# Kernel optimization log

Hardware: AMD Instinct MI355X
Metric: run time of the kernel (lower is better)

Reference implementation:

```python
import jax, jax.numpy as jnp
import numpy as np

B, T, IN, HID = 256, 512, 1024, 1024


def setup_inputs() -> dict:
    key = jax.random.key(0)
    ks = jax.random.split(key, 9)
    s = 1.0 / np.sqrt(IN + HID)
    def lin(k):
        kw, kb = jax.random.split(k)
        W = jax.random.uniform(kw, (IN + HID, HID), jnp.float32, -s, s)
        b = jax.random.uniform(kb, (HID,), jnp.float32, -s, s)
        return W, b
    Wf, bf = lin(ks[0])
    Wi, bi = lin(ks[1])
    Wo, bo = lin(ks[2])
    Wc, bc = lin(ks[3])
    x = jax.random.normal(ks[4], (B, T, IN), jnp.float32)
    return {"x": x, "Wf": Wf, "bf": bf, "Wi": Wi, "bi": bi,
            "Wo": Wo, "bo": bo, "Wc": Wc, "bc": bc}


def reference(x, Wf, bf, Wi, bi, Wo, bo, Wc, bc):
    # x: [B, T, IN]; returns final (h, c): each [B, HID]
    batch = x.shape[0]
    hid = Wf.shape[1]

    def step(carry, xt):
        h, c = carry
        comb = jnp.concatenate([xt, h], axis=1)      # [B, IN+HID]
        i = jax.nn.sigmoid(comb @ Wi + bi)
        f = jax.nn.sigmoid(comb @ Wf + bf)
        o = jax.nn.sigmoid(comb @ Wo + bo)
        g = jnp.tanh(comb @ Wc + bc)
        c_next = f * c + i * g
        h_next = o * jnp.tanh(c_next)
        return (h_next, c_next), None

    init = (jnp.zeros((batch, hid), x.dtype), jnp.zeros((batch, hid), x.dtype))
    (h, c), _ = jax.lax.scan(step, init, jnp.swapaxes(x, 0, 1))
    return (h, c)
```

## Files before the change

### kernel.cpp

```cpp
#include <hip/hip_runtime.h>
#include <hip/hip_bf16.h>
#include <hip/hip_cooperative_groups.h>

#define B_DIM 256
#define T_DIM 512
#define IN_DIM 1024
#define HID_DIM 1024
#define BLK 16384

typedef __attribute__((ext_vector_type(8))) short bf16x8;
typedef __attribute__((ext_vector_type(4))) float f32x4;

__device__ __forceinline__ unsigned short f2bf(float v) {
  unsigned int u = __float_as_uint(v);
  unsigned int r = (u + 0x7fffu + ((u >> 16) & 1u)) >> 16;
  return (unsigned short)r;
}

typedef __attribute__((address_space(3))) unsigned int lds_uint;
typedef const __attribute__((address_space(1))) unsigned int g_uint;
__device__ __forceinline__ void gload_lds16(const void* g, void* l) {
  __builtin_amdgcn_global_load_lds((g_uint*)g, (lds_uint*)l, 16, 0, 0);
}

__device__ __forceinline__ void glds4(const unsigned char* s, unsigned char* d) {
#pragma unroll
  for (int i = 0; i < 4; ++i) gload_lds16(s + i * 1024, d + i * 1024);
}

__device__ __forceinline__ void h_load(unsigned long long (&r)[8],
                                       const unsigned char* src) {
#pragma unroll
  for (int p = 0; p < 8; ++p)
    r[p] = __hip_atomic_load((const unsigned long long*)(src + p * 512),
                             __ATOMIC_RELAXED, __HIP_MEMORY_SCOPE_AGENT);
}

__device__ __forceinline__ void h_write(unsigned long long (&r)[8],
                                        unsigned char* dst) {
#pragma unroll
  for (int p = 0; p < 8; ++p)
    *(unsigned long long*)(dst + p * 512) = r[p];
  asm volatile("s_waitcnt lgkmcnt(0)" ::: "memory");
}

__device__ __forceinline__ void spin_ge(unsigned int* p, unsigned int tgt) {
  while (__hip_atomic_fetch_add(p, 0u, __ATOMIC_RELAXED,
                                __HIP_MEMORY_SCOPE_AGENT) < tgt)
    __builtin_amdgcn_s_sleep(8);
  asm volatile("" ::: "memory");
}

__global__ void prep_pack_w(const float* __restrict__ Wi, const float* __restrict__ Wf,
                            const float* __restrict__ Wo, const float* __restrict__ Wc,
                            unsigned char* __restrict__ Wp) {
  const int bid = blockIdx.x;
  const int cb = bid >> 4, kc = bid & 15;
  const int tid = threadIdx.x;
  const int col = tid & 63;
  const int g = col >> 4, h_in = col & 15;
  const int kq = tid >> 6;
  const float* W = (g == 0) ? Wi : (g == 1) ? Wf : (g == 2) ? Wo : Wc;
  const float* src = W + (size_t)(kc * 128 + kq * 32) * HID_DIM + cb * 16 + h_in;
  unsigned char* dst = Wp + (size_t)bid * BLK;
  const unsigned int xo = (unsigned int)((col & 7) << 4);
#pragma unroll
  for (int b4 = 0; b4 < 4; ++b4) {
    unsigned short u[8];
#pragma unroll
    for (int j = 0; j < 8; ++j)
      u[j] = f2bf(src[(size_t)(b4 * 8 + j) * HID_DIM]);
    uint4 pk;
    pk.x = (unsigned)u[0] | ((unsigned)u[1] << 16);
    pk.y = (unsigned)u[2] | ((unsigned)u[3] << 16);
    pk.z = (unsigned)u[4] | ((unsigned)u[5] << 16);
    pk.w = (unsigned)u[6] | ((unsigned)u[7] << 16);
    unsigned int byte = ((unsigned int)(col * 256 + kq * 64 + b4 * 16)) ^ xo;
    *(uint4*)(dst + byte) = pk;
  }
}

__global__ void prep_bias(const float* __restrict__ bi, const float* __restrict__ bf_,
                          const float* __restrict__ bo, const float* __restrict__ bc,
                          float* __restrict__ bp) {
  int p = blockIdx.x * 256 + threadIdx.x;
  int cbb = p >> 6, col = p & 63, g = col >> 4, h_in = col & 15;
  const float* b = (g == 0) ? bi : (g == 1) ? bf_ : (g == 2) ? bo : bc;
  bp[p] = b[cbb * 16 + h_in];
}

__global__ void prep_pack_x(const float* __restrict__ x, unsigned char* __restrict__ xp) {
  const int bid = blockIdx.x;
  const int kc = bid & 7, mb = (bid >> 3) & 3, t = bid >> 5;
  const int tid = threadIdx.x;
  const int row = tid >> 2, kseg = tid & 3;
  const float* src = x + ((size_t)(mb * 64 + row) * T_DIM + t) * IN_DIM + kc * 128 + kseg * 32;
  unsigned char* dst = xp + (size_t)bid * BLK;
  const unsigned int xo = (unsigned)((row & 7) << 4);
#pragma unroll
  for (int c4 = 0; c4 < 4; ++c4) {
    float4 f0 = *(const float4*)(src + c4 * 8);
    float4 f1 = *(const float4*)(src + c4 * 8 + 4);
    uint4 pk;
    pk.x = (unsigned)f2bf(f0.x) | ((unsigned)f2bf(f0.y) << 16);
    pk.y = (unsigned)f2bf(f0.z) | ((unsigned)f2bf(f0.w) << 16);
    pk.z = (unsigned)f2bf(f1.x) | ((unsigned)f2bf(f1.y) << 16);
    pk.w = (unsigned)f2bf(f1.z) | ((unsigned)f2bf(f1.w) << 16);
    *(uint4*)(dst + (((unsigned)(row * 256 + kseg * 64 + c4 * 16)) ^ xo)) = pk;
  }
}

__global__ __launch_bounds__(512, 1) void lstm_persist(
    const unsigned char* __restrict__ xp, const unsigned char* __restrict__ Wq,
    const float* __restrict__ bp, unsigned char* hring,
    unsigned int* prodCnt, unsigned int* consCnt, float* __restrict__ out) {
  extern __shared__ unsigned char ring[];
  const int wg = blockIdx.x, mb = wg >> 6, cb = wg & 63;
  const int tid = threadIdx.x, lane = tid & 63, w = tid >> 6;
  const int wr = w >> 2, wc = w & 3;
  const int fr = lane & 15;
  const unsigned koff2 = (unsigned)((lane >> 4) << 4);

  const int erow = tid & 63, hb2 = (tid >> 6) * 2;
  float bI[2], bF[2], bO[2], bG[2];
#pragma unroll
  for (int j = 0; j < 2; ++j) {
    bI[j] = bp[cb * 64 + hb2 + j];
    bF[j] = bp[cb * 64 + 16 + hb2 + j];
    bO[j] = bp[cb * 64 + 32 + hb2 + j];
    bG[j] = bp[cb * 64 + 48 + hb2 + j];
  }
  float cr[2] = {0.f, 0.f};

  const unsigned char* WB = Wq + (size_t)(cb * 16) * BLK;
  unsigned long long hA[8], hB[8];

#pragma unroll 1
  for (int t = 0; t < T_DIM; ++t) {
    const int NC = (t == 0) ? 8 : 16;
    const unsigned char* xA =
        xp + ((size_t)(t * 4 + mb)) * (8 * BLK) + w * 4096 + lane * 16;
    const unsigned char* hSrc =
        hring + (size_t)((t + 2) % 3) * 524288 +
        (size_t)(mb * 8) * BLK + w * 4096 + lane * 8;

    f32x4 acc[2] = {{0.f, 0.f, 0.f, 0.f}, {0.f, 0.f, 0.f, 0.f}};

    auto consume = [&](int buf) {
      const unsigned char* Ab = ring + buf * 32768;
      const unsigned char* Bb = Ab + BLK;
#pragma unroll
      for (int ks = 0; ks < 4; ++ks) {
        const unsigned kb2 = (unsigned)ks * 64 + koff2;
        const unsigned r0 = (unsigned)(wr * 32 + fr), r1 = r0 + 16;
        const unsigned cl = (unsigned)(wc * 16 + fr);
        bf16x8 a0 = *(const bf16x8*)(Ab + ((r0 * 256 + kb2) ^ ((r0 & 7) << 4)));
        bf16x8 a1 = *(const bf16x8*)(Ab + ((r1 * 256 + kb2) ^ ((r1 & 7) << 4)));
        bf16x8 b0 = *(const bf16x8*)(Bb + ((cl * 256 + kb2) ^ ((cl & 7) << 4)));
        acc[0] = __builtin_amdgcn_mfma_f32_16x16x32_bf16(a0, b0, acc[0], 0, 0, 0);
        acc[1] = __builtin_amdgcn_mfma_f32_16x16x32_bf16(a1, b0, acc[1], 0, 0, 0);
      }
    };

    if (w < 4) {
#pragma unroll
      for (int c = 0; c < 3; ++c)
        glds4(xA + (size_t)c * BLK, ring + c * 32768 + (w << 12));
    } else {
#pragma unroll
      for (int c = 0; c < 3; ++c)
        glds4(WB + (size_t)c * BLK + ((w - 4) << 12) + lane * 16,
              ring + c * 32768 + BLK + ((w - 4) << 12));
    }

#pragma unroll 1
    for (int kc = 0; kc < NC; ++kc) {
      const int nx = kc + 3;
      const bool isq = nx < NC;
      if (isq && nx == 8) {
        if (lane == 0) spin_ge(&prodCnt[(t - 1) * 4 + mb], 64u);
        __builtin_amdgcn_sched_barrier(0);
      }
      if (w < 4) {
        if (isq && nx < 8)
          glds4(xA + (size_t)nx * BLK, ring + (nx & 3) * 32768 + (w << 12));
        if (kc + 1 >= 8 && kc + 1 < NC) {
          unsigned char* d = ring + ((kc + 1) & 3) * 32768 + (w << 12) + lane * 8;
          if (((kc + 1) & 1) == 0) h_write(hA, d);
          else h_write(hB, d);
        }
        if (isq && nx >= 8) {
          const unsigned char* s = hSrc + (size_t)(nx - 8) * BLK;
          if ((nx & 1) == 0) h_load(hA, s);
          else h_load(hB, s);
        }
      } else {
        if (isq)
          glds4(WB + (size_t)nx * BLK + ((w - 4) << 12) + lane * 16,
                ring + (nx & 3) * 32768 + BLK + ((w - 4) << 12));
      }
      const int ahead = NC - 1 - kc;
      if (ahead >= 3)      asm volatile("s_waitcnt vmcnt(12)" ::: "memory");
      else if (ahead == 2) asm volatile("s_waitcnt vmcnt(8)" ::: "memory");
      else if (ahead == 1) asm volatile("s_waitcnt vmcnt(4)" ::: "memory");
      else                 asm volatile("s_waitcnt vmcnt(0)" ::: "memory");
      __builtin_amdgcn_s_barrier();
      consume(kc & 3);
      __builtin_amdgcn_s_barrier();
    }

    float* gates = (float*)ring;
#pragma unroll
    for (int m = 0; m < 2; ++m)
#pragma unroll
      for (int j = 0; j < 4; ++j) {
        int row = wr * 32 + m * 16 + (lane >> 4) * 4 + j;
        int col = wc * 16 + fr;
        gates[row * 65 + col] = acc[m][j];
      }
    __syncthreads();

    float hv[2];
#pragma unroll
    for (int j = 0; j < 2; ++j) {
      int hc = hb2 + j;
      float pi = gates[erow * 65 + hc] + bI[j];
      float pf = gates[erow * 65 + 16 + hc] + bF[j];
      float po = gates[erow * 65 + 32 + hc] + bO[j];
      float pg = gates[erow * 65 + 48 + hc] + bG[j];
      float ig = 1.f / (1.f + __expf(-pi));
      float fg = 1.f / (1.f + __expf(-pf));
      float og = 1.f / (1.f + __expf(-po));
      float gg = 1.f - 2.f / (1.f + __expf(2.f * pg));
      float cn = fg * cr[j] + ig * gg;
      cr[j] = cn;
      hv[j] = og * (1.f - 2.f / (1.f + __expf(2.f * cn)));
    }

    if (t >= 3) {
      if (tid == 0) spin_ge(&consCnt[(t - 2) * 4 + mb], 64u);
      __syncthreads();
    }
    if (t < T_DIM - 1) {
      int hcg = cb * 16 + hb2;
      int kc2 = hcg >> 7, kp = hcg & 127;
      unsigned byte = ((unsigned)(erow * 256 + kp * 2)) ^ ((unsigned)((erow & 7) << 4));
      unsigned pk = (unsigned)f2bf(hv[0]) | ((unsigned)f2bf(hv[1]) << 16);
      unsigned int* hd = (unsigned int*)(hring + (size_t)(t % 3) * 524288 +
                                         (size_t)(mb * 8 + kc2) * BLK + byte);
      __hip_atomic_store(hd, pk, __ATOMIC_RELAXED, __HIP_MEMORY_SCOPE_AGENT);
    }
    asm volatile("s_waitcnt vmcnt(0)" ::: "memory");
    __syncthreads();
    if (tid == 0) {
      if (t < T_DIM - 1)
        __hip_atomic_fetch_add(&prodCnt[t * 4 + mb], 1u, __ATOMIC_RELEASE,
                               __HIP_MEMORY_SCOPE_AGENT);
      if (t >= 1)
        __hip_atomic_fetch_add(&consCnt[t * 4 + mb], 1u, __ATOMIC_RELAXED,
                               __HIP_MEMORY_SCOPE_AGENT);
    }
    if (t == T_DIM - 1) {
      size_t gidx = (size_t)(mb * 64 + erow) * HID_DIM + cb * 16 + hb2;
      *(float2*)(out + gidx) = make_float2(hv[0], hv[1]);
      *(float2*)(out + (size_t)B_DIM * HID_DIM + gidx) = make_float2(cr[0], cr[1]);
    }
  }
}

extern "C" void kernel_launch(void* const* d_in, const int* in_sizes, int n_in,
                              void* d_out, int out_size, void* d_ws, size_t ws_size,
                              hipStream_t stream) {
  (void)in_sizes; (void)n_in; (void)out_size;
  const float* x   = (const float*)d_in[0];
  const float* Wf_ = (const float*)d_in[1];
  const float* bf_ = (const float*)d_in[2];
  const float* Wi_ = (const float*)d_in[3];
  const float* bi_ = (const float*)d_in[4];
  const float* Wo_ = (const float*)d_in[5];
  const float* bo_ = (const float*)d_in[6];
  const float* Wc_ = (const float*)d_in[7];
  const float* bc_ = (const float*)d_in[8];

  unsigned char* ws = (unsigned char*)d_ws;
  unsigned char* Wp = ws;
  size_t off = 16777216;
  float* bp = (float*)(ws + off);          off += 16384;
  unsigned int* prodCnt = (unsigned int*)(ws + off); off += 8192;
  unsigned int* consCnt = (unsigned int*)(ws + off); off += 8192;
  unsigned char* hring = ws + off;         off += 3 * 524288;
  unsigned char* xpp = ws + off;           off += 268435456;
  if (ws_size < off) return;
  float* out = (float*)d_out;

  prep_pack_w<<<1024, 256, 0, stream>>>(Wi_, Wf_, Wo_, Wc_, Wp);
  prep_bias<<<16, 256, 0, stream>>>(bi_, bf_, bo_, bc_, bp);
  prep_pack_x<<<16384, 256, 0, stream>>>(x, xpp);
  hipMemsetAsync(prodCnt, 0, 16384, stream);

  hipFuncSetAttribute((const void*)lstm_persist,
                      hipFuncAttributeMaxDynamicSharedMemorySize, 131072);
  const unsigned char* a_xp = xpp;
  const unsigned char* a_wp = Wp;
  const float* a_bp = bp;
  unsigned char* a_hr = hring;
  unsigned int* a_pc = prodCnt;
  unsigned int* a_cc = consCnt;
  float* a_out = out;
  void* args[] = {&a_xp, &a_wp, &a_bp, &a_hr, &a_pc, &a_cc, &a_out};
  hipLaunchCooperativeKernel((const void*)lstm_persist, dim3(256), dim3(512),
                             args, 131072u, stream);
}
```

Baseline: 11.14 ms.

## Warp-specialize LSTM: register-resident weights, x-projection one step ahead of recurrence

Adds a new persistent kernel that splits each workgroup's waves into two roles. Four waves compute the recurrent h·W_h product, and four waves compute the next timestep's x·W_x product and hand it over through a double-buffered global gx buffer. The weight slices stay in registers for the whole run instead of being streamed from memory every step. This takes the input projection off the serial critical path, so each step's dependent work covers only the hidden-state half of K. In exchange it uses more registers, adds a global round trip for the partial gate sums, and shortens the spin sleep. The old kernel is kept as a fallback for when the workspace is too small.

```diff
diff --git a/kernel.cpp b/kernel.cpp
--- a/kernel.cpp
+++ b/kernel.cpp
@@ -1,6 +1,5 @@
 #include <hip/hip_runtime.h>
 #include <hip/hip_bf16.h>
-#include <hip/hip_cooperative_groups.h>
 
 #define B_DIM 256
 #define T_DIM 512
@@ -22,33 +21,25 @@
 __device__ __forceinline__ void gload_lds16(const void* g, void* l) {
   __builtin_amdgcn_global_load_lds((g_uint*)g, (lds_uint*)l, 16, 0, 0);
 }
-
 __device__ __forceinline__ void glds4(const unsigned char* s, unsigned char* d) {
 #pragma unroll
   for (int i = 0; i < 4; ++i) gload_lds16(s + i * 1024, d + i * 1024);
-}
-
-__device__ __forceinline__ void h_load(unsigned long long (&r)[8],
-                                       const unsigned char* src) {
-#pragma unroll
-  for (int p = 0; p < 8; ++p)
-    r[p] = __hip_atomic_load((const unsigned long long*)(src + p * 512),
-                             __ATOMIC_RELAXED, __HIP_MEMORY_SCOPE_AGENT);
-}
-
-__device__ __forceinline__ void h_write(unsigned long long (&r)[8],
-                                        unsigned char* dst) {
-#pragma unroll
-  for (int p = 0; p < 8; ++p)
-    *(unsigned long long*)(dst + p * 512) = r[p];
-  asm volatile("s_waitcnt lgkmcnt(0)" ::: "memory");
 }
 
 __device__ __forceinline__ void spin_ge(unsigned int* p, unsigned int tgt) {
   while (__hip_atomic_fetch_add(p, 0u, __ATOMIC_RELAXED,
                                 __HIP_MEMORY_SCOPE_AGENT) < tgt)
-    __builtin_amdgcn_s_sleep(8);
+    __builtin_amdgcn_s_sleep(2);
   asm volatile("" ::: "memory");
+}
+
+__device__ __forceinline__ void waitvm(int n) {
+  switch (n) {
+    case 12: asm volatile("s_waitcnt vmcnt(12)" ::: "memory"); break;
+    case 8:  asm volatile("s_waitcnt vmcnt(8)" ::: "memory"); break;
+    case 4:  asm volatile("s_waitcnt vmcnt(4)" ::: "memory"); break;
+    default: asm volatile("s_waitcnt vmcnt(0)" ::: "memory"); break;
+  }
 }
 
 __global__ void prep_pack_w(const float* __restrict__ Wi, const float* __restrict__ Wf,
@@ -110,6 +101,193 @@
   }
 }
 
+__global__ __launch_bounds__(512, 2) void lstm_ws(
+    const unsigned char* __restrict__ xp, const unsigned char* __restrict__ Wq,
+    const float* __restrict__ bp, float* gx, unsigned char* hring,
+    unsigned int* prodCnt, unsigned int* consCnt, float* __restrict__ out) {
+  extern __shared__ unsigned char ring[];
+  const int wg = blockIdx.x, mb = wg >> 6, cb = wg & 63;
+  const int tid = threadIdx.x, lane = tid & 63, w = tid >> 6;
+  const bool isH = (w < 4);
+  const int wq = w & 3;
+  const int fr = lane & 15;
+  const unsigned koff2 = (unsigned)((lane >> 4) << 4);
+  const int cl = wq * 16 + fr;
+  const int rsub = (lane >> 4) * 4;
+
+  bf16x8 Breg[8][4];
+  {
+    const int hx = isH ? 8 : 0;
+#pragma unroll
+    for (int kcl = 0; kcl < 8; ++kcl)
+#pragma unroll
+      for (int ks = 0; ks < 4; ++ks)
+        Breg[kcl][ks] = *(const bf16x8*)(
+            Wq + ((size_t)(cb * 16 + hx + kcl) << 14) +
+            (((unsigned)(cl * 256 + ks * 64 + koff2)) ^ ((unsigned)((cl & 7) << 4))));
+  }
+  const int erow = tid & 63, hb2 = (tid >> 6) * 2;
+  float bI[2], bF[2], bO[2], bG[2];
+#pragma unroll
+  for (int j = 0; j < 2; ++j) {
+    bI[j] = bp[cb * 64 + hb2 + j];
+    bF[j] = bp[cb * 64 + 16 + hb2 + j];
+    bO[j] = bp[cb * 64 + 32 + hb2 + j];
+    bG[j] = bp[cb * 64 + 48 + hb2 + j];
+  }
+  float cr[2] = {0.f, 0.f};
+
+  unsigned char* hbufs = ring;
+  unsigned char* xbufs = ring + 65536;
+  float* gates = (float*)ring;
+
+#pragma unroll 1
+  for (int t = -1; t < T_DIM; ++t) {
+    const bool hAct = isH && (t >= 1);
+    const bool xAct = (!isH) && (t < T_DIM - 1);
+
+    f32x4 acc[4] = {{0.f, 0.f, 0.f, 0.f}, {0.f, 0.f, 0.f, 0.f},
+                    {0.f, 0.f, 0.f, 0.f}, {0.f, 0.f, 0.f, 0.f}};
+    if (isH && t >= 0) {
+      const float* gt = gx + (size_t)(t & 1) * 1048576 + (size_t)wg * 4096;
+#pragma unroll
+      for (int rb = 0; rb < 4; ++rb)
+#pragma unroll
+        for (int j = 0; j < 4; ++j)
+          acc[rb][j] = gt[(rb * 16 + rsub + j) * 64 + cl];
+    }
+    if (hAct) {
+      if (lane == 0) {
+        spin_ge(&prodCnt[(t - 1) * 4 + mb], 64u);
+        (void)__hip_atomic_load(&prodCnt[(t - 1) * 4 + mb], __ATOMIC_ACQUIRE,
+                                __HIP_MEMORY_SCOPE_AGENT);
+      }
+      __builtin_amdgcn_sched_barrier(0);
+    }
+    const unsigned char* hA = hring + (size_t)((t + 2) % 3) * 524288 +
+                              (size_t)(mb * 8) * BLK + wq * 4096 + lane * 16;
+    const unsigned char* xA = xp + ((size_t)((t + 1) * 4 + mb)) * (8 * BLK) +
+                              wq * 4096 + lane * 16;
+    if (hAct) {
+#pragma unroll
+      for (int c = 0; c < 3; ++c)
+        glds4(hA + (size_t)c * BLK, hbufs + c * 16384 + wq * 4096);
+    }
+    if (xAct) {
+#pragma unroll
+      for (int c = 0; c < 3; ++c)
+        glds4(xA + (size_t)c * BLK, xbufs + c * 16384 + wq * 4096);
+    }
+#pragma unroll
+    for (int kc = 0; kc < 8; ++kc) {
+      if (kc < 5) {
+        if (hAct)
+          glds4(hA + (size_t)(kc + 3) * BLK, hbufs + ((kc + 3) & 3) * 16384 + wq * 4096);
+        if (xAct)
+          glds4(xA + (size_t)(kc + 3) * BLK, xbufs + ((kc + 3) & 3) * 16384 + wq * 4096);
+      }
+      waitvm(kc < 5 ? 12 : (kc == 5 ? 8 : (kc == 6 ? 4 : 0)));
+      __builtin_amdgcn_s_barrier();
+      if (hAct || xAct) {
+        const unsigned char* Ab = (isH ? hbufs : xbufs) + (kc & 3) * 16384;
+#pragma unroll
+        for (int ks = 0; ks < 4; ++ks) {
+          const unsigned kb2 = (unsigned)ks * 64 + koff2;
+#pragma unroll
+          for (int rb = 0; rb < 4; ++rb) {
+            const unsigned row = (unsigned)(rb * 16 + fr);
+            bf16x8 a = *(const bf16x8*)(Ab + ((row * 256 + kb2) ^ ((row & 7) << 4)));
+            acc[rb] = __builtin_amdgcn_mfma_f32_16x16x32_bf16(a, Breg[kc][ks], acc[rb], 0, 0, 0);
+          }
+        }
+      }
+      __builtin_amdgcn_s_barrier();
+    }
+
+    if (isH && t >= 0) {
+#pragma unroll
+      for (int rb = 0; rb < 4; ++rb)
+#pragma unroll
+        for (int j = 0; j < 4; ++j)
+          gates[(rb * 16 + rsub + j) * 65 + cl] = acc[rb][j];
+    }
+    if (xAct) {
+      float* gt = gx + (size_t)((t + 1) & 1) * 1048576 + (size_t)wg * 4096;
+#pragma unroll
+      for (int rb = 0; rb < 4; ++rb)
+#pragma unroll
+        for (int j = 0; j < 4; ++j)
+          __hip_atomic_store(&gt[(rb * 16 + rsub + j) * 64 + cl], acc[rb][j],
+                             __ATOMIC_RELAXED, __HIP_MEMORY_SCOPE_AGENT);
+    }
+    if (t >= 0) {
+      __syncthreads();
+      float hv[2];
+#pragma unroll
+      for (int j = 0; j < 2; ++j) {
+        int hc = hb2 + j;
+        float pi = gates[erow * 65 + hc] + bI[j];
+        float pf = gates[erow * 65 + 16 + hc] + bF[j];
+        float po = gates[erow * 65 + 32 + hc] + bO[j];
+        float pg = gates[erow * 65 + 48 + hc] + bG[j];
+        float ig = 1.f / (1.f + __expf(-pi));
+        float fg = 1.f / (1.f + __expf(-pf));
+        float og = 1.f / (1.f + __expf(-po));
+        float gg = 1.f - 2.f / (1.f + __expf(2.f * pg));
+        float cn = fg * cr[j] + ig * gg;
+        cr[j] = cn;
+        hv[j] = og * (1.f - 2.f / (1.f + __expf(2.f * cn)));
+      }
+      if (t >= 3) {
+        if (tid == 0) spin_ge(&consCnt[(t - 2) * 4 + mb], 64u);
+        __syncthreads();
+      }
+      if (t < T_DIM - 1) {
+        int hcg = cb * 16 + hb2;
+        int kc2 = hcg >> 7, kp = hcg & 127;
+        unsigned byte = ((unsigned)(erow * 256 + kp * 2)) ^ ((unsigned)((erow & 7) << 4));
+        unsigned pk = (unsigned)f2bf(hv[0]) | ((unsigned)f2bf(hv[1]) << 16);
+        unsigned int* hd = (unsigned int*)(hring + (size_t)(t % 3) * 524288 +
+                                           (size_t)(mb * 8 + kc2) * BLK + byte);
+        __hip_atomic_store(hd, pk, __ATOMIC_RELAXED, __HIP_MEMORY_SCOPE_AGENT);
+      }
+      asm volatile("s_waitcnt vmcnt(0)" ::: "memory");
+      __syncthreads();
+      if (tid == 0) {
+        if (t < T_DIM - 1)
+          __hip_atomic_fetch_add(&prodCnt[t * 4 + mb], 1u, __ATOMIC_RELEASE,
+                                 __HIP_MEMORY_SCOPE_AGENT);
+        if (t >= 1)
+          __hip_atomic_fetch_add(&consCnt[t * 4 + mb], 1u, __ATOMIC_RELAXED,
+                                 __HIP_MEMORY_SCOPE_AGENT);
+      }
+      if (t == T_DIM - 1) {
+        size_t gidx = (size_t)(mb * 64 + erow) * HID_DIM + cb * 16 + hb2;
+        *(float2*)(out + gidx) = make_float2(hv[0], hv[1]);
+        *(float2*)(out + (size_t)B_DIM * HID_DIM + gidx) = make_float2(cr[0], cr[1]);
+      }
+    } else {
+      asm volatile("s_waitcnt vmcnt(0)" ::: "memory");
+      __syncthreads();
+    }
+  }
+}
+
+__device__ __forceinline__ void h_load_fb(unsigned long long (&r)[8],
+                                          const unsigned char* src) {
+#pragma unroll
+  for (int p = 0; p < 8; ++p)
+    r[p] = __hip_atomic_load((const unsigned long long*)(src + p * 512),
+                             __ATOMIC_RELAXED, __HIP_MEMORY_SCOPE_AGENT);
+}
+__device__ __forceinline__ void h_write_fb(unsigned long long (&r)[8],
+                                           unsigned char* dst) {
+#pragma unroll
+  for (int p = 0; p < 8; ++p)
+    *(unsigned long long*)(dst + p * 512) = r[p];
+  asm volatile("s_waitcnt lgkmcnt(0)" ::: "memory");
+}
+
 __global__ __launch_bounds__(512, 1) void lstm_persist(
     const unsigned char* __restrict__ xp, const unsigned char* __restrict__ Wq,
     const float* __restrict__ bp, unsigned char* hring,
@@ -120,7 +298,6 @@
   const int wr = w >> 2, wc = w & 3;
   const int fr = lane & 15;
   const unsigned koff2 = (unsigned)((lane >> 4) << 4);
-
   const int erow = tid & 63, hb2 = (tid >> 6) * 2;
   float bI[2], bF[2], bO[2], bG[2];
 #pragma unroll
@@ -131,7 +308,6 @@
     bG[j] = bp[cb * 64 + 48 + hb2 + j];
   }
   float cr[2] = {0.f, 0.f};
-
   const unsigned char* WB = Wq + (size_t)(cb * 16) * BLK;
   unsigned long long hA[8], hB[8];
 
@@ -143,9 +319,7 @@
     const unsigned char* hSrc =
         hring + (size_t)((t + 2) % 3) * 524288 +
         (size_t)(mb * 8) * BLK + w * 4096 + lane * 8;
-
     f32x4 acc[2] = {{0.f, 0.f, 0.f, 0.f}, {0.f, 0.f, 0.f, 0.f}};
-
     auto consume = [&](int buf) {
       const unsigned char* Ab = ring + buf * 32768;
       const unsigned char* Bb = Ab + BLK;
@@ -153,15 +327,14 @@
       for (int ks = 0; ks < 4; ++ks) {
         const unsigned kb2 = (unsigned)ks * 64 + koff2;
         const unsigned r0 = (unsigned)(wr * 32 + fr), r1 = r0 + 16;
-        const unsigned cl = (unsigned)(wc * 16 + fr);
+        const unsigned clx = (unsigned)(wc * 16 + fr);
         bf16x8 a0 = *(const bf16x8*)(Ab + ((r0 * 256 + kb2) ^ ((r0 & 7) << 4)));
         bf16x8 a1 = *(const bf16x8*)(Ab + ((r1 * 256 + kb2) ^ ((r1 & 7) << 4)));
-        bf16x8 b0 = *(const bf16x8*)(Bb + ((cl * 256 + kb2) ^ ((cl & 7) << 4)));
+        bf16x8 b0 = *(const bf16x8*)(Bb + ((clx * 256 + kb2) ^ ((clx & 7) << 4)));
         acc[0] = __builtin_amdgcn_mfma_f32_16x16x32_bf16(a0, b0, acc[0], 0, 0, 0);
         acc[1] = __builtin_amdgcn_mfma_f32_16x16x32_bf16(a1, b0, acc[1], 0, 0, 0);
       }
     };
-
     if (w < 4) {
 #pragma unroll
       for (int c = 0; c < 3; ++c)
@@ -172,7 +345,6 @@
         glds4(WB + (size_t)c * BLK + ((w - 4) << 12) + lane * 16,
               ring + c * 32768 + BLK + ((w - 4) << 12));
     }
-
 #pragma unroll 1
     for (int kc = 0; kc < NC; ++kc) {
       const int nx = kc + 3;
@@ -186,13 +358,13 @@
           glds4(xA + (size_t)nx * BLK, ring + (nx & 3) * 32768 + (w << 12));
         if (kc + 1 >= 8 && kc + 1 < NC) {
           unsigned char* d = ring + ((kc + 1) & 3) * 32768 + (w << 12) + lane * 8;
-          if (((kc + 1) & 1) == 0) h_write(hA, d);
-          else h_write(hB, d);
+          if (((kc + 1) & 1) == 0) h_write_fb(hA, d);
+          else h_write_fb(hB, d);
         }
         if (isq && nx >= 8) {
           const unsigned char* s = hSrc + (size_t)(nx - 8) * BLK;
-          if ((nx & 1) == 0) h_load(hA, s);
-          else h_load(hB, s);
+          if ((nx & 1) == 0) h_load_fb(hA, s);
+          else h_load_fb(hB, s);
         }
       } else {
         if (isq)
@@ -208,7 +380,6 @@
       consume(kc & 3);
       __builtin_amdgcn_s_barrier();
     }
-
     float* gates = (float*)ring;
 #pragma unroll
     for (int m = 0; m < 2; ++m)
@@ -219,7 +390,6 @@
         gates[row * 65 + col] = acc[m][j];
       }
     __syncthreads();
-
     float hv[2];
 #pragma unroll
     for (int j = 0; j < 2; ++j) {
@@ -236,7 +406,6 @@
       cr[j] = cn;
       hv[j] = og * (1.f - 2.f / (1.f + __expf(2.f * cn)));
     }
-
     if (t >= 3) {
       if (tid == 0) spin_ge(&consCnt[(t - 2) * 4 + mb], 64u);
       __syncthreads();
@@ -281,33 +450,52 @@
   const float* bo_ = (const float*)d_in[6];
   const float* Wc_ = (const float*)d_in[7];
   const float* bc_ = (const float*)d_in[8];
-
+  float* out = (float*)d_out;
   unsigned char* ws = (unsigned char*)d_ws;
+
   unsigned char* Wp = ws;
   size_t off = 16777216;
-  float* bp = (float*)(ws + off);          off += 16384;
+  float* bp = (float*)(ws + off);                    off += 16384;
   unsigned int* prodCnt = (unsigned int*)(ws + off); off += 8192;
   unsigned int* consCnt = (unsigned int*)(ws + off); off += 8192;
-  unsigned char* hring = ws + off;         off += 3 * 524288;
-  unsigned char* xpp = ws + off;           off += 268435456;
-  if (ws_size < off) return;
-  float* out = (float*)d_out;
+  unsigned char* hring = ws + off;                   off += 3 * 524288;
+  float* gxr = (float*)(ws + off);                   off += 2 * 4194304;
+  unsigned char* xpp = ws + off;                     off += 268435456;
+  const size_t NEED_NEW = off;
 
   prep_pack_w<<<1024, 256, 0, stream>>>(Wi_, Wf_, Wo_, Wc_, Wp);
   prep_bias<<<16, 256, 0, stream>>>(bi_, bf_, bo_, bc_, bp);
-  prep_pack_x<<<16384, 256, 0, stream>>>(x, xpp);
   hipMemsetAsync(prodCnt, 0, 16384, stream);
 
-  hipFuncSetAttribute((const void*)lstm_persist,
-                      hipFuncAttributeMaxDynamicSharedMemorySize, 131072);
-  const unsigned char* a_xp = xpp;
-  const unsigned char* a_wp = Wp;
-  const float* a_bp = bp;
-  unsigned char* a_hr = hring;
-  unsigned int* a_pc = prodCnt;
-  unsigned int* a_cc = consCnt;
-  float* a_out = out;
-  void* args[] = {&a_xp, &a_wp, &a_bp, &a_hr, &a_pc, &a_cc, &a_out};
-  hipLaunchCooperativeKernel((const void*)lstm_persist, dim3(256), dim3(512),
-                             args, 131072u, stream);
-}
+  if (ws_size >= NEED_NEW) {
+    prep_pack_x<<<16384, 256, 0, stream>>>(x, xpp);
+    hipFuncSetAttribute((const void*)lstm_ws,
+                        hipFuncAttributeMaxDynamicSharedMemorySize, 131072);
+    const unsigned char* a_xp = xpp;
+    const unsigned char* a_wp = Wp;
+    const float* a_bp = bp;
+    float* a_gx = gxr;
+    unsigned char* a_hr = hring;
+    unsigned int* a_pc = prodCnt;
+    unsigned int* a_cc = consCnt;
+    float* a_out = out;
+    void* args[] = {&a_xp, &a_wp, &a_bp, &a_gx, &a_hr, &a_pc, &a_cc, &a_out};
+    hipLaunchCooperativeKernel((const void*)lstm_ws, dim3(256), dim3(512),
+                               args, 131072u, stream);
+  } else {
+    unsigned char* xpp3 = ws + (NEED_NEW - 268435456 - 2 * 4194304);
+    prep_pack_x<<<16384, 256, 0, stream>>>(x, xpp3);
+    hipFuncSetAttribute((const void*)lstm_persist,
+                        hipFuncAttributeMaxDynamicSharedMemorySize, 131072);
+    const unsigned char* a_xp = xpp3;
+    const unsigned char* a_wp = Wp;
+    const float* a_bp = bp;
+    unsigned char* a_hr = hring;
+    unsigned int* a_pc = prodCnt;
+    unsigned int* a_cc = consCnt;
+    float* a_out = out;
+    void* args[] = {&a_xp, &a_wp, &a_bp, &a_hr, &a_pc, &a_cc, &a_out};
+    hipLaunchCooperativeKernel((const void*)lstm_persist, dim3(256), dim3(512),
+                               args, 131072u, stream);
+  }
+}
```

Measured after the change: 17.79 ms. +59.7%, slower.

## Hoist input projection into windowed bulk GEMM and keep recurrent weights in registers

Applied to the files above, without the earlier changes.

Splits the LSTM into time windows. In each window a parallel bulk_gx kernel precomputes the x@W input-gate contributions for all steps and stores them as bf16. A persistent lstm_seq kernel then does only the h@W recurrent half per step, with weight slices held in registers instead of streamed from global memory every step. This removes half the serial-path GEMM work and the per-step weight traffic. In exchange it adds extra kernel launches per window, storage of precomputed gates in bf16 (more rounding), and carrying the cell state across launches.

```diff
diff --git a/kernel.cpp b/kernel.cpp
--- a/kernel.cpp
+++ b/kernel.cpp
@@ -1,9 +1,9 @@
 #include <hip/hip_runtime.h>
 #include <hip/hip_bf16.h>
-#include <hip/hip_cooperative_groups.h>
 
 #define B_DIM 256
 #define T_DIM 512
+#define WINT 64
 #define IN_DIM 1024
 #define HID_DIM 1024
 #define BLK 16384
@@ -16,40 +16,27 @@
   unsigned int r = (u + 0x7fffu + ((u >> 16) & 1u)) >> 16;
   return (unsigned short)r;
 }
+__device__ __forceinline__ float bflo(unsigned u) { return __uint_as_float(u << 16); }
+__device__ __forceinline__ float bfhi(unsigned u) { return __uint_as_float(u & 0xffff0000u); }
 
 typedef __attribute__((address_space(3))) unsigned int lds_uint;
 typedef const __attribute__((address_space(1))) unsigned int g_uint;
 __device__ __forceinline__ void gload_lds16(const void* g, void* l) {
   __builtin_amdgcn_global_load_lds((g_uint*)g, (lds_uint*)l, 16, 0, 0);
 }
-
-__device__ __forceinline__ void glds4(const unsigned char* s, unsigned char* d) {
-#pragma unroll
-  for (int i = 0; i < 4; ++i) gload_lds16(s + i * 1024, d + i * 1024);
-}
-
-__device__ __forceinline__ void h_load(unsigned long long (&r)[8],
-                                       const unsigned char* src) {
-#pragma unroll
-  for (int p = 0; p < 8; ++p)
-    r[p] = __hip_atomic_load((const unsigned long long*)(src + p * 512),
-                             __ATOMIC_RELAXED, __HIP_MEMORY_SCOPE_AGENT);
-}
-
-__device__ __forceinline__ void h_write(unsigned long long (&r)[8],
-                                        unsigned char* dst) {
-#pragma unroll
-  for (int p = 0; p < 8; ++p)
-    *(unsigned long long*)(dst + p * 512) = r[p];
-  asm volatile("s_waitcnt lgkmcnt(0)" ::: "memory");
+__device__ __forceinline__ void glds2(const unsigned char* s, unsigned char* d) {
+  gload_lds16(s, d);
+  gload_lds16(s + 1024, d + 1024);
 }
 
 __device__ __forceinline__ void spin_ge(unsigned int* p, unsigned int tgt) {
   while (__hip_atomic_fetch_add(p, 0u, __ATOMIC_RELAXED,
                                 __HIP_MEMORY_SCOPE_AGENT) < tgt)
-    __builtin_amdgcn_s_sleep(8);
+    __builtin_amdgcn_s_sleep(2);
   asm volatile("" ::: "memory");
 }
+
+#define WAITVM(N) asm volatile("s_waitcnt vmcnt(" #N ")" ::: "memory")
 
 __global__ void prep_pack_w(const float* __restrict__ Wi, const float* __restrict__ Wf,
                             const float* __restrict__ Wo, const float* __restrict__ Wc,
@@ -89,13 +76,15 @@
   bp[p] = b[cbb * 16 + h_in];
 }
 
-__global__ void prep_pack_x(const float* __restrict__ x, unsigned char* __restrict__ xp) {
+__global__ void prep_pack_x_win(const float* __restrict__ x,
+                                unsigned char* __restrict__ xpw, int t0) {
   const int bid = blockIdx.x;
-  const int kc = bid & 7, mb = (bid >> 3) & 3, t = bid >> 5;
+  const int kc = bid & 7, mb = (bid >> 3) & 3, tw = bid >> 5;
   const int tid = threadIdx.x;
   const int row = tid >> 2, kseg = tid & 3;
-  const float* src = x + ((size_t)(mb * 64 + row) * T_DIM + t) * IN_DIM + kc * 128 + kseg * 32;
-  unsigned char* dst = xp + (size_t)bid * BLK;
+  const float* src = x + ((size_t)(mb * 64 + row) * T_DIM + (t0 + tw)) * IN_DIM +
+                     kc * 128 + kseg * 32;
+  unsigned char* dst = xpw + (size_t)bid * BLK;
   const unsigned int xo = (unsigned)((row & 7) << 4);
 #pragma unroll
   for (int c4 = 0; c4 < 4; ++c4) {
@@ -110,18 +99,139 @@
   }
 }
 
-__global__ __launch_bounds__(512, 1) void lstm_persist(
-    const unsigned char* __restrict__ xp, const unsigned char* __restrict__ Wq,
+__global__ __launch_bounds__(512, 2) void bulk_gx(
+    const unsigned char* __restrict__ xpw, const unsigned char* __restrict__ Wq,
+    unsigned char* __restrict__ gxw) {
+  extern __shared__ unsigned char ring[];
+  const int wg = blockIdx.x;
+  const int cb = wg & 63, mb = (wg >> 6) & 3, tg = wg >> 8;
+  const int tid = threadIdx.x, lane = tid & 63, w = tid >> 6;
+  const int rg = w & 1, cg = (w >> 1) & 1, kh = w >> 2;
+  const int fr = lane & 15;
+  const unsigned koff2 = (unsigned)((lane >> 4) << 4);
+  const int rsub = (lane >> 4) * 4;
+  const int cl = cg * 32 + fr;
+
+  bf16x8 Breg[4][2][4];
+#pragma unroll
+  for (int ci = 0; ci < 4; ++ci)
+#pragma unroll
+    for (int cbf = 0; cbf < 2; ++cbf)
+#pragma unroll
+      for (int ks = 0; ks < 4; ++ks) {
+        const unsigned c2 = (unsigned)(cl + cbf * 16);
+        Breg[ci][cbf][ks] = *(const bf16x8*)(
+            Wq + ((size_t)(cb * 16 + kh * 4 + ci) << 14) +
+            ((c2 * 256 + (unsigned)ks * 64 + koff2) ^ ((c2 & 7) << 4)));
+      }
+
+  float* gates = (float*)ring;
+  unsigned char* dstb = ring + w * 2048;
+
+#pragma unroll 1
+  for (int i = 0; i < 16; ++i) {
+    const int tl = tg * 16 + i;
+    const unsigned char* xA =
+        xpw + ((size_t)((tl * 4 + mb) * 8)) * BLK + w * 2048 + lane * 16;
+    f32x4 acc[2][2] = {{{0.f,0.f,0.f,0.f},{0.f,0.f,0.f,0.f}},
+                       {{0.f,0.f,0.f,0.f},{0.f,0.f,0.f,0.f}}};
+#pragma unroll
+    for (int c = 0; c < 4; ++c) glds2(xA + (size_t)c * BLK, dstb + c * 16384);
+#pragma unroll
+    for (int kc = 0; kc < 8; ++kc) {
+      if (kc <= 4) WAITVM(6);
+      else if (kc == 5) WAITVM(4);
+      else if (kc == 6) WAITVM(2);
+      else WAITVM(0);
+      __builtin_amdgcn_s_barrier();
+      if ((kc >> 2) == kh) {
+        const unsigned char* Ab = ring + (kc & 3) * 16384;
+#pragma unroll
+        for (int ks = 0; ks < 4; ++ks) {
+          const unsigned r0 = (unsigned)(rg * 32 + fr), r1 = r0 + 16;
+          const unsigned kb = (unsigned)ks * 64 + koff2;
+          bf16x8 a0 = *(const bf16x8*)(Ab + ((r0 * 256 + kb) ^ ((r0 & 7) << 4)));
+          bf16x8 a1 = *(const bf16x8*)(Ab + ((r1 * 256 + kb) ^ ((r1 & 7) << 4)));
+#pragma unroll
+          for (int cbf = 0; cbf < 2; ++cbf) {
+            acc[0][cbf] = __builtin_amdgcn_mfma_f32_16x16x32_bf16(
+                a0, Breg[kc & 3][cbf][ks], acc[0][cbf], 0, 0, 0);
+            acc[1][cbf] = __builtin_amdgcn_mfma_f32_16x16x32_bf16(
+                a1, Breg[kc & 3][cbf][ks], acc[1][cbf], 0, 0, 0);
+          }
+        }
+      }
+      __builtin_amdgcn_s_barrier();
+      if (kc + 4 < 8) glds2(xA + (size_t)(kc + 4) * BLK, dstb + ((kc + 4) & 3) * 16384);
+    }
+    if (kh == 0) {
+#pragma unroll
+      for (int rb = 0; rb < 2; ++rb)
+#pragma unroll
+        for (int cbf = 0; cbf < 2; ++cbf)
+#pragma unroll
+          for (int j = 0; j < 4; ++j)
+            gates[(rg * 32 + rb * 16 + rsub + j) * 65 + cg * 32 + cbf * 16 + fr] =
+                acc[rb][cbf][j];
+    }
+    __syncthreads();
+    if (kh == 1) {
+#pragma unroll
+      for (int rb = 0; rb < 2; ++rb)
+#pragma unroll
+        for (int cbf = 0; cbf < 2; ++cbf)
+#pragma unroll
+          for (int j = 0; j < 4; ++j)
+            gates[(rg * 32 + rb * 16 + rsub + j) * 65 + cg * 32 + cbf * 16 + fr] +=
+                acc[rb][cbf][j];
+    }
+    __syncthreads();
+    {
+      const int erow = tid & 63, hb2 = (tid >> 6) * 2;
+      uint4 pk;
+      unsigned u[4];
+#pragma unroll
+      for (int g = 0; g < 4; ++g) {
+        float lo = gates[erow * 65 + g * 16 + hb2];
+        float hi = gates[erow * 65 + g * 16 + hb2 + 1];
+        u[g] = (unsigned)f2bf(lo) | ((unsigned)f2bf(hi) << 16);
+      }
+      pk.x = u[0]; pk.y = u[1]; pk.z = u[2]; pk.w = u[3];
+      *(uint4*)(gxw + ((size_t)((tl * 4 + mb) * 64 + cb)) * 8192 + (size_t)tid * 16) = pk;
+    }
+    __syncthreads();
+  }
+}
+
+__global__ __launch_bounds__(512, 2) void lstm_seq(
+    const unsigned char* __restrict__ gxw, const unsigned char* __restrict__ Wq,
     const float* __restrict__ bp, unsigned char* hring,
-    unsigned int* prodCnt, unsigned int* consCnt, float* __restrict__ out) {
+    unsigned int* prodCnt, unsigned int* consCnt, float* cst,
+    float* __restrict__ out, int t0) {
   extern __shared__ unsigned char ring[];
   const int wg = blockIdx.x, mb = wg >> 6, cb = wg & 63;
   const int tid = threadIdx.x, lane = tid & 63, w = tid >> 6;
-  const int wr = w >> 2, wc = w & 3;
+  const int rg = w & 1, cg = (w >> 1) & 1, kh = w >> 2;
   const int fr = lane & 15;
   const unsigned koff2 = (unsigned)((lane >> 4) << 4);
+  const int rsub = (lane >> 4) * 4;
+  const int cl = cg * 32 + fr;
+
+  bf16x8 Breg[4][2][4];
+#pragma unroll
+  for (int ci = 0; ci < 4; ++ci)
+#pragma unroll
+    for (int cbf = 0; cbf < 2; ++cbf)
+#pragma unroll
+      for (int ks = 0; ks < 4; ++ks) {
+        const unsigned c2 = (unsigned)(cl + cbf * 16);
+        Breg[ci][cbf][ks] = *(const bf16x8*)(
+            Wq + ((size_t)(cb * 16 + 8 + kh * 4 + ci) << 14) +
+            ((c2 * 256 + (unsigned)ks * 64 + koff2) ^ ((c2 & 7) << 4)));
+      }
 
   const int erow = tid & 63, hb2 = (tid >> 6) * 2;
+  const size_t gidx = (size_t)(mb * 64 + erow) * HID_DIM + cb * 16 + hb2;
   float bI[2], bF[2], bO[2], bG[2];
 #pragma unroll
   for (int j = 0; j < 2; ++j) {
@@ -131,112 +241,102 @@
     bG[j] = bp[cb * 64 + 48 + hb2 + j];
   }
   float cr[2] = {0.f, 0.f};
-
-  const unsigned char* WB = Wq + (size_t)(cb * 16) * BLK;
-  unsigned long long hA[8], hB[8];
+  if (t0 > 0) { float2 c2v = *(const float2*)(cst + gidx); cr[0] = c2v.x; cr[1] = c2v.y; }
+
+  float* gates = (float*)ring;
+  unsigned char* dstb = ring + w * 2048;
 
 #pragma unroll 1
-  for (int t = 0; t < T_DIM; ++t) {
-    const int NC = (t == 0) ? 8 : 16;
-    const unsigned char* xA =
-        xp + ((size_t)(t * 4 + mb)) * (8 * BLK) + w * 4096 + lane * 16;
-    const unsigned char* hSrc =
-        hring + (size_t)((t + 2) % 3) * 524288 +
-        (size_t)(mb * 8) * BLK + w * 4096 + lane * 8;
-
-    f32x4 acc[2] = {{0.f, 0.f, 0.f, 0.f}, {0.f, 0.f, 0.f, 0.f}};
-
-    auto consume = [&](int buf) {
-      const unsigned char* Ab = ring + buf * 32768;
-      const unsigned char* Bb = Ab + BLK;
-#pragma unroll
-      for (int ks = 0; ks < 4; ++ks) {
-        const unsigned kb2 = (unsigned)ks * 64 + koff2;
-        const unsigned r0 = (unsigned)(wr * 32 + fr), r1 = r0 + 16;
-        const unsigned cl = (unsigned)(wc * 16 + fr);
-        bf16x8 a0 = *(const bf16x8*)(Ab + ((r0 * 256 + kb2) ^ ((r0 & 7) << 4)));
-        bf16x8 a1 = *(const bf16x8*)(Ab + ((r1 * 256 + kb2) ^ ((r1 & 7) << 4)));
-        bf16x8 b0 = *(const bf16x8*)(Bb + ((cl * 256 + kb2) ^ ((cl & 7) << 4)));
-        acc[0] = __builtin_amdgcn_mfma_f32_16x16x32_bf16(a0, b0, acc[0], 0, 0, 0);
-        acc[1] = __builtin_amdgcn_mfma_f32_16x16x32_bf16(a1, b0, acc[1], 0, 0, 0);
-      }
-    };
-
-    if (w < 4) {
-#pragma unroll
-      for (int c = 0; c < 3; ++c)
-        glds4(xA + (size_t)c * BLK, ring + c * 32768 + (w << 12));
-    } else {
-#pragma unroll
-      for (int c = 0; c < 3; ++c)
-        glds4(WB + (size_t)c * BLK + ((w - 4) << 12) + lane * 16,
-              ring + c * 32768 + BLK + ((w - 4) << 12));
-    }
-
-#pragma unroll 1
-    for (int kc = 0; kc < NC; ++kc) {
-      const int nx = kc + 3;
-      const bool isq = nx < NC;
-      if (isq && nx == 8) {
-        if (lane == 0) spin_ge(&prodCnt[(t - 1) * 4 + mb], 64u);
-        __builtin_amdgcn_sched_barrier(0);
-      }
-      if (w < 4) {
-        if (isq && nx < 8)
-          glds4(xA + (size_t)nx * BLK, ring + (nx & 3) * 32768 + (w << 12));
-        if (kc + 1 >= 8 && kc + 1 < NC) {
-          unsigned char* d = ring + ((kc + 1) & 3) * 32768 + (w << 12) + lane * 8;
-          if (((kc + 1) & 1) == 0) h_write(hA, d);
-          else h_write(hB, d);
+  for (int tt = 0; tt < WINT; ++tt) {
+    const int t = t0 + tt;
+    uint4 gxv = *(const uint4*)(gxw + ((size_t)((tt * 4 + mb) * 64 + cb)) * 8192 +
+                                (size_t)tid * 16);
+    f32x4 acc[2][2] = {{{0.f,0.f,0.f,0.f},{0.f,0.f,0.f,0.f}},
+                       {{0.f,0.f,0.f,0.f},{0.f,0.f,0.f,0.f}}};
+    if (t > 0) {
+      if (lane == 0) {
+        spin_ge(&prodCnt[(t - 1) * 4 + mb], 64u);
+        (void)__hip_atomic_load(&prodCnt[(t - 1) * 4 + mb], __ATOMIC_ACQUIRE,
+                                __HIP_MEMORY_SCOPE_AGENT);
+      }
+      __builtin_amdgcn_sched_barrier(0);
+      const unsigned char* hA = hring + (size_t)((t + 2) % 3) * 524288 +
+                                (size_t)(mb * 8) * BLK + w * 2048 + lane * 16;
+#pragma unroll
+      for (int c = 0; c < 4; ++c) glds2(hA + (size_t)c * BLK, dstb + c * 16384);
+#pragma unroll
+      for (int kc = 0; kc < 8; ++kc) {
+        if (kc <= 4) WAITVM(6);
+        else if (kc == 5) WAITVM(4);
+        else if (kc == 6) WAITVM(2);
+        else WAITVM(0);
+        __builtin_amdgcn_s_barrier();
+        if ((kc >> 2) == kh) {
+          const unsigned char* Ab = ring + (kc & 3) * 16384;
+#pragma unroll
+          for (int ks = 0; ks < 4; ++ks) {
+            const unsigned r0 = (unsigned)(rg * 32 + fr), r1 = r0 + 16;
+            const unsigned kb = (unsigned)ks * 64 + koff2;
+            bf16x8 a0 = *(const bf16x8*)(Ab + ((r0 * 256 + kb) ^ ((r0 & 7) << 4)));
+            bf16x8 a1 = *(const bf16x8*)(Ab + ((r1 * 256 + kb) ^ ((r1 & 7) << 4)));
+#pragma unroll
+            for (int cbf = 0; cbf < 2; ++cbf) {
+              acc[0][cbf] = __builtin_amdgcn_mfma_f32_16x16x32_bf16(
+                  a0, Breg[kc & 3][cbf][ks], acc[0][cbf], 0, 0, 0);
+              acc[1][cbf] = __builtin_amdgcn_mfma_f32_16x16x32_bf16(
+                  a1, Breg[kc & 3][cbf][ks], acc[1][cbf], 0, 0, 0);
+            }
+          }
         }
-        if (isq && nx >= 8) {
-          const unsigned char* s = hSrc + (size_t)(nx - 8) * BLK;
-          if ((nx & 1) == 0) h_load(hA, s);
-          else h_load(hB, s);
-        }
-      } else {
-        if (isq)
-          glds4(WB + (size_t)nx * BLK + ((w - 4) << 12) + lane * 16,
-                ring + (nx & 3) * 32768 + BLK + ((w - 4) << 12));
-      }
-      const int ahead = NC - 1 - kc;
-      if (ahead >= 3)      asm volatile("s_waitcnt vmcnt(12)" ::: "memory");
-      else if (ahead == 2) asm volatile("s_waitcnt vmcnt(8)" ::: "memory");
-      else if (ahead == 1) asm volatile("s_waitcnt vmcnt(4)" ::: "memory");
-      else                 asm volatile("s_waitcnt vmcnt(0)" ::: "memory");
-      __builtin_amdgcn_s_barrier();
-      consume(kc & 3);
-      __builtin_amdgcn_s_barrier();
-    }
-
-    float* gates = (float*)ring;
-#pragma unroll
-    for (int m = 0; m < 2; ++m)
-#pragma unroll
-      for (int j = 0; j < 4; ++j) {
-        int row = wr * 32 + m * 16 + (lane >> 4) * 4 + j;
-        int col = wc * 16 + fr;
-        gates[row * 65 + col] = acc[m][j];
-      }
-    __syncthreads();
-
+        __builtin_amdgcn_s_barrier();
+        if (kc + 4 < 8) glds2(hA + (size_t)(kc + 4) * BLK, dstb + ((kc + 4) & 3) * 16384);
+      }
+    }
+    if (kh == 0) {
+#pragma unroll
+      for (int rb = 0; rb < 2; ++rb)
+#pragma unroll
+        for (int cbf = 0; cbf < 2; ++cbf)
+#pragma unroll
+          for (int j = 0; j < 4; ++j)
+            gates[(rg * 32 + rb * 16 + rsub + j) * 65 + cg * 32 + cbf * 16 + fr] =
+                acc[rb][cbf][j];
+    }
+    __syncthreads();
+    if (kh == 1) {
+#pragma unroll
+      for (int rb = 0; rb < 2; ++rb)
+#pragma unroll
+        for (int cbf = 0; cbf < 2; ++cbf)
+#pragma unroll
+          for (int j = 0; j < 4; ++j)
+            gates[(rg * 32 + rb * 16 + rsub + j) * 65 + cg * 32 + cbf * 16 + fr] +=
+                acc[rb][cbf][j];
+    }
+    __syncthreads();
     float hv[2];
-#pragma unroll
-    for (int j = 0; j < 2; ++j) {
-      int hc = hb2 + j;
-      float pi = gates[erow * 65 + hc] + bI[j];
-      float pf = gates[erow * 65 + 16 + hc] + bF[j];
-      float po = gates[erow * 65 + 32 + hc] + bO[j];
-      float pg = gates[erow * 65 + 48 + hc] + bG[j];
-      float ig = 1.f / (1.f + __expf(-pi));
-      float fg = 1.f / (1.f + __expf(-pf));
-      float og = 1.f / (1.f + __expf(-po));
-      float gg = 1.f - 2.f / (1.f + __expf(2.f * pg));
-      float cn = fg * cr[j] + ig * gg;
-      cr[j] = cn;
-      hv[j] = og * (1.f - 2.f / (1.f + __expf(2.f * cn)));
-    }
-
+    {
+      unsigned gu0 = gxv.x, gu1 = gxv.y, gu2 = gxv.z, gu3 = gxv.w;
+#pragma unroll
+      for (int j = 0; j < 2; ++j) {
+        int hc = hb2 + j;
+        float gx0 = j ? bfhi(gu0) : bflo(gu0);
+        float gx1 = j ? bfhi(gu1) : bflo(gu1);
+        float gx2 = j ? bfhi(gu2) : bflo(gu2);
+        float gx3 = j ? bfhi(gu3) : bflo(gu3);
+        float pi = gates[erow * 65 + hc]      + bI[j] + gx0;
+        float pf = gates[erow * 65 + 16 + hc] + bF[j] + gx1;
+        float po = gates[erow * 65 + 32 + hc] + bO[j] + gx2;
+        float pg = gates[erow * 65 + 48 + hc] + bG[j] + gx3;
+        float ig = 1.f / (1.f + __expf(-pi));
+        float fg = 1.f / (1.f + __expf(-pf));
+        float og = 1.f / (1.f + __expf(-po));
+        float gg = 1.f - 2.f / (1.f + __expf(2.f * pg));
+        float cn = fg * cr[j] + ig * gg;
+        cr[j] = cn;
+        hv[j] = og * (1.f - 2.f / (1.f + __expf(2.f * cn)));
+      }
+    }
     if (t >= 3) {
       if (tid == 0) spin_ge(&consCnt[(t - 2) * 4 + mb], 64u);
       __syncthreads();
@@ -250,7 +350,7 @@
                                          (size_t)(mb * 8 + kc2) * BLK + byte);
       __hip_atomic_store(hd, pk, __ATOMIC_RELAXED, __HIP_MEMORY_SCOPE_AGENT);
     }
-    asm volatile("s_waitcnt vmcnt(0)" ::: "memory");
+    WAITVM(0);
     __syncthreads();
     if (tid == 0) {
       if (t < T_DIM - 1)
@@ -261,11 +361,11 @@
                                __HIP_MEMORY_SCOPE_AGENT);
     }
     if (t == T_DIM - 1) {
-      size_t gidx = (size_t)(mb * 64 + erow) * HID_DIM + cb * 16 + hb2;
       *(float2*)(out + gidx) = make_float2(hv[0], hv[1]);
       *(float2*)(out + (size_t)B_DIM * HID_DIM + gidx) = make_float2(cr[0], cr[1]);
     }
   }
+  if (t0 + WINT < T_DIM) *(float2*)(cst + gidx) = make_float2(cr[0], cr[1]);
 }
 
 extern "C" void kernel_launch(void* const* d_in, const int* in_sizes, int n_in,
@@ -281,33 +381,43 @@
   const float* bo_ = (const float*)d_in[6];
   const float* Wc_ = (const float*)d_in[7];
   const float* bc_ = (const float*)d_in[8];
-
+  float* out = (float*)d_out;
   unsigned char* ws = (unsigned char*)d_ws;
+
   unsigned char* Wp = ws;
   size_t off = 16777216;
-  float* bp = (float*)(ws + off);          off += 16384;
+  float* bp = (float*)(ws + off);                    off += 16384;
   unsigned int* prodCnt = (unsigned int*)(ws + off); off += 8192;
   unsigned int* consCnt = (unsigned int*)(ws + off); off += 8192;
-  unsigned char* hring = ws + off;         off += 3 * 524288;
-  unsigned char* xpp = ws + off;           off += 268435456;
+  unsigned char* hring = ws + off;                   off += 3 * 524288;
+  float* cst = (float*)(ws + off);                   off += 1048576;
+  unsigned char* xpw = ws + off;                     off += (size_t)2048 * BLK;
+  unsigned char* gxw = ws + off;                     off += (size_t)WINT * 256 * 8192;
   if (ws_size < off) return;
-  float* out = (float*)d_out;
 
   prep_pack_w<<<1024, 256, 0, stream>>>(Wi_, Wf_, Wo_, Wc_, Wp);
   prep_bias<<<16, 256, 0, stream>>>(bi_, bf_, bo_, bc_, bp);
-  prep_pack_x<<<16384, 256, 0, stream>>>(x, xpp);
   hipMemsetAsync(prodCnt, 0, 16384, stream);
 
-  hipFuncSetAttribute((const void*)lstm_persist,
-                      hipFuncAttributeMaxDynamicSharedMemorySize, 131072);
-  const unsigned char* a_xp = xpp;
-  const unsigned char* a_wp = Wp;
-  const float* a_bp = bp;
-  unsigned char* a_hr = hring;
-  unsigned int* a_pc = prodCnt;
-  unsigned int* a_cc = consCnt;
-  float* a_out = out;
-  void* args[] = {&a_xp, &a_wp, &a_bp, &a_hr, &a_pc, &a_cc, &a_out};
-  hipLaunchCooperativeKernel((const void*)lstm_persist, dim3(256), dim3(512),
-                             args, 131072u, stream);
-}
+  hipFuncSetAttribute((const void*)bulk_gx,
+                      hipFuncAttributeMaxDynamicSharedMemorySize, 65536);
+  hipFuncSetAttribute((const void*)lstm_seq,
+                      hipFuncAttributeMaxDynamicSharedMemorySize, 65536);
+
+  for (int t0 = 0; t0 < T_DIM; t0 += WINT) {
+    prep_pack_x_win<<<2048, 256, 0, stream>>>(x, xpw, t0);
+    bulk_gx<<<1024, 512, 65536, stream>>>(xpw, Wp, gxw);
+    const unsigned char* a_gx = gxw;
+    const unsigned char* a_wp = Wp;
+    const float* a_bp = bp;
+    unsigned char* a_hr = hring;
+    unsigned int* a_pc = prodCnt;
+    unsigned int* a_cc = consCnt;
+    float* a_cs = cst;
+    float* a_out = out;
+    int a_t0 = t0;
+    void* args[] = {&a_gx, &a_wp, &a_bp, &a_hr, &a_pc, &a_cc, &a_cs, &a_out, &a_t0};
+    hipLaunchCooperativeKernel((const void*)lstm_seq, dim3(256), dim3(512),
+                               args, 65536u, stream);
+  }
+}
```

Result: slower. 26.06 ms (+133.9%).
